# Performance work log

Hardware: AMD Instinct MI355X
Metric: run time of the kernel (lower is better)

The kernel has to match this reference:

```python
import jax, jax.numpy as jnp
import numpy as np

B, S, D, H = 2, 2048, 1024, 16
DK = D // H

def setup_inputs() -> dict:
    key = jax.random.key(0)
    ks = jax.random.split(key, 8)
    scale = 1.0 / np.sqrt(D)
    return {
        "q": jax.random.normal(ks[0], (B, S, D), jnp.float32),
        "k": jax.random.normal(ks[1], (B, S, D), jnp.float32),
        "v": jax.random.normal(ks[2], (B, S, D), jnp.float32),
        "reaches": jax.random.uniform(ks[3], (B, S), jnp.float32),
        "Wq": jax.random.normal(ks[4], (D, D), jnp.float32) * scale,
        "Wk": jax.random.normal(ks[5], (D, D), jnp.float32) * scale,
        "Wv": jax.random.normal(ks[6], (D, D), jnp.float32) * scale,
        "Wo": jax.random.normal(ks[7], (D, D), jnp.float32) * scale,
    }

def _split_heads(x):
    # [B,S,D] -> [B,H,S,DK]
    return x.reshape(B, S, H, DK).transpose(0, 2, 1, 3)

def reference(q, k, v, reaches, Wq, Wk, Wv, Wo):
    # torch Linear: y = x @ W.T
    qh = _split_heads(q @ Wq.T)
    kh = _split_heads(k @ Wk.T)
    vh = _split_heads(v @ Wv.T)
    scores = jnp.einsum("bhqd,bhkd->bhqk", qh, kh) / jnp.sqrt(jnp.float32(DK))
    scores = jax.nn.softmax(scores, axis=-1)
    # post-softmax reach weighting along key axis
    scores = scores * reaches[:, None, None, :]
    # diagonal suppression: scores - scores*0.999999*eye
    scores = scores * (1.0 - 0.999999 * jnp.eye(S, dtype=scores.dtype))
    # inverted combine
    out = vh - jnp.einsum("bhqk,bhkd->bhqd", scores, vh)
    # per-position contribution rescale
    rs = reaches.sum(axis=-1, keepdims=True)
    contrib = (rs - reaches) / (rs + 1e-9) * (1.0 - reaches) * 100.0  # [B,S]
    out = out * contrib[:, None, :, None]
    concat = out.transpose(0, 2, 1, 3).reshape(B, S, D)
    return concat @ Wo.T
```

## Files before the change

### kernel.cpp

```cpp
#include <hip/hip_runtime.h>
#include <hip/hip_bf16.h>

typedef __attribute__((ext_vector_type(8))) short short8;
typedef __attribute__((ext_vector_type(4))) float f32x4;
typedef __attribute__((ext_vector_type(16))) float f32x16;
typedef unsigned short us;

#define B_ 2
#define S_ 2048
#define D_ 1024
#define H_ 16
#define DK_ 64
#define QSCALE 0.1803368867f

__device__ __forceinline__ us f2bf(float f) {
  union { float f; unsigned u; } x; x.f = f;
  unsigned r = x.u + 0x7FFFu + ((x.u >> 16) & 1u);
  return (us)(r >> 16);
}
__device__ __forceinline__ float bf2f(us h) {
  union { unsigned u; float f; } x; x.u = ((unsigned)h) << 16;
  return x.f;
}
__device__ __forceinline__ us f2bf_hw(float f) {
  __hip_bfloat16 h = __float2bfloat16(f);
  return *reinterpret_cast<us*>(&h);
}
__device__ __forceinline__ unsigned cvtpk(float lo, float hi) {
  unsigned r;
  asm("v_cvt_pk_bf16_f32 %0, %1, %2" : "=v"(r) : "v"(lo), "v"(hi));
  return r;
}

__device__ __forceinline__ void gload16(const void* g, void* l) {
  __builtin_amdgcn_global_load_lds((const __attribute__((address_space(1))) void*)g,
                                   (__attribute__((address_space(3))) void*)l, 16, 0, 0);
}

__global__ __launch_bounds__(256) void cvt_all(const float* __restrict__ q,
                                               const float* __restrict__ k,
                                               const float* __restrict__ v,
                                               const float* __restrict__ Wq,
                                               const float* __restrict__ Wk,
                                               const float* __restrict__ Wv,
                                               const float* __restrict__ Wo,
                                               us* __restrict__ oq, us* __restrict__ ok,
                                               us* __restrict__ ov, us* __restrict__ oWq,
                                               us* __restrict__ oWk, us* __restrict__ oWv,
                                               us* __restrict__ oWo) {
  int bid = blockIdx.x;
  const float* in; us* out; int off;
  if (bid < 12288) {
    int t = bid >> 12;
    in = (t == 0) ? q : (t == 1) ? k : v;
    out = (t == 0) ? oq : (t == 1) ? ok : ov;
    off = (bid & 4095) * 1024;
  } else {
    int t = (bid - 12288) >> 10;
    in = (t == 0) ? Wq : (t == 1) ? Wk : (t == 2) ? Wv : Wo;
    out = (t == 0) ? oWq : (t == 1) ? oWk : (t == 2) ? oWv : oWo;
    off = ((bid - 12288) & 1023) * 1024;
  }
  int i = off + threadIdx.x * 4;
  float4 val = *reinterpret_cast<const float4*>(in + i);
  ushort4 o;
  o.x = f2bf(val.x); o.y = f2bf(val.y); o.z = f2bf(val.z); o.w = f2bf(val.w);
  *reinterpret_cast<ushort4*>(out + i) = o;
}

__global__ __launch_bounds__(256) void rs_kernel(const float* __restrict__ reaches,
                                                 float* __restrict__ rs) {
  int b = blockIdx.x, t = threadIdx.x;
  float s = 0.f;
  for (int i = t; i < S_; i += 256) s += reaches[b * S_ + i];
  for (int o = 32; o > 0; o >>= 1) s += __shfl_down(s, o, 64);
  __shared__ float tmp[4];
  if ((t & 63) == 0) tmp[t >> 6] = s;
  __syncthreads();
  if (t == 0) rs[b] = tmp[0] + tmp[1] + tmp[2] + tmp[3];
}

__device__ __forceinline__ void gemm_core_hs(const us* __restrict__ A, const us* __restrict__ Bt,
                                             us* __restrict__ outH, float oscale) {
  __shared__ __align__(16) us lA[3][128 * 32];
  __shared__ __align__(16) us lB[3][128 * 32];
  const int tid = threadIdx.x;
  const int bm = blockIdx.x >> 3, bn = blockIdx.x & 7;
  const int w = tid >> 6, lane = tid & 63;
  const int wr = (w >> 1) * 64, wc = (w & 1) * 64;
  const int lr = lane & 15, lg = lane >> 4;

  f32x4 acc[4][4];
#pragma unroll
  for (int i = 0; i < 4; ++i)
#pragma unroll
    for (int j = 0; j < 4; ++j) acc[i][j] = (f32x4){0.f, 0.f, 0.f, 0.f};

  const int crow = lane >> 2, ce8 = (lane & 3) * 8;
  const us* A0 = A + (size_t)(bm * 128 + w * 32 + crow) * 1024 + ce8;
  const us* A1 = A0 + (size_t)16 * 1024;
  const us* B0 = Bt + (size_t)(bn * 128 + w * 32 + crow) * 1024 + ce8;
  const us* B1 = B0 + (size_t)16 * 1024;
  const int dA0 = (w * 32) * 32, dA1 = (w * 32 + 16) * 32;

  gload16(A0, &lA[0][dA0]);
  gload16(A1, &lA[0][dA1]);
  gload16(B0, &lB[0][dA0]);
  gload16(B1, &lB[0][dA1]);

  int cur = 0, nxt = 1;
  for (int kt = 0; kt < 32; ++kt) {
    if (kt < 31) {
      int ko = (kt + 1) * 32;
      gload16(A0 + ko, &lA[nxt][dA0]);
      gload16(A1 + ko, &lA[nxt][dA1]);
      gload16(B0 + ko, &lB[nxt][dA0]);
      gload16(B1 + ko, &lB[nxt][dA1]);
      asm volatile("s_waitcnt vmcnt(4)" ::: "memory");
    } else {
      asm volatile("s_waitcnt vmcnt(0)" ::: "memory");
    }
    __builtin_amdgcn_s_barrier();
    __builtin_amdgcn_sched_barrier(0);

    short8 af[4], bfr[4];
#pragma unroll
    for (int i = 0; i < 4; ++i)
      af[i] = *reinterpret_cast<const short8*>(&lA[cur][(wr + i * 16 + lr) * 32 + lg * 8]);
#pragma unroll
    for (int j = 0; j < 4; ++j)
      bfr[j] = *reinterpret_cast<const short8*>(&lB[cur][(wc + j * 16 + lr) * 32 + lg * 8]);
    __builtin_amdgcn_s_setprio(1);
#pragma unroll
    for (int i = 0; i < 4; ++i)
#pragma unroll
      for (int j = 0; j < 4; ++j)
        acc[i][j] = __builtin_amdgcn_mfma_f32_16x16x32_bf16(af[i], bfr[j], acc[i][j], 0, 0, 0);
    __builtin_amdgcn_s_setprio(0);

    cur = nxt;
    nxt = (nxt == 2) ? 0 : nxt + 1;
  }
#pragma unroll
  for (int i = 0; i < 4; ++i)
#pragma unroll
    for (int j = 0; j < 4; ++j)
#pragma unroll
      for (int ii = 0; ii < 4; ++ii) {
        int r = bm * 128 + wr + i * 16 + lg * 4 + ii;
        int c = bn * 128 + wc + j * 16 + lr;
        float v = acc[i][j][ii] * oscale;
        int b = r >> 11, s = r & (S_ - 1), h = c >> 6, dk = c & 63;
        outH[(((size_t)(b * H_ + h) * S_ + s) * DK_) + dk] = f2bf(v);
      }
}

__global__ __launch_bounds__(256) void proj_gemm(const us* __restrict__ q_bf,
                                                 const us* __restrict__ k_bf,
                                                 const us* __restrict__ v_bf,
                                                 const us* __restrict__ Wq_bf,
                                                 const us* __restrict__ Wk_bf,
                                                 const us* __restrict__ Wv_bf,
                                                 us* __restrict__ Qh, us* __restrict__ Kh,
                                                 us* __restrict__ Vh) {
  if (blockIdx.y == 0) gemm_core_hs(q_bf, Wq_bf, Qh, QSCALE);
  else if (blockIdx.y == 1) gemm_core_hs(k_bf, Wk_bf, Kh, 1.0f);
  else gemm_core_hs(v_bf, Wv_bf, Vh, 1.0f);
}

__global__ __launch_bounds__(256) void wo_gemm(const us* __restrict__ A,
                                               const us* __restrict__ Bt,
                                               float* __restrict__ outF) {
  __shared__ __align__(16) us lA[3][128 * 32];
  __shared__ __align__(16) us lB[3][64 * 32];
  const int tid = threadIdx.x;
  const int bm = blockIdx.x >> 4, bn = blockIdx.x & 15;
  const int w = tid >> 6, lane = tid & 63;
  const int lr = lane & 15, lg = lane >> 4;

  f32x4 acc[2][4];
#pragma unroll
  for (int i = 0; i < 2; ++i)
#pragma unroll
    for (int j = 0; j < 4; ++j) acc[i][j] = (f32x4){0.f, 0.f, 0.f, 0.f};

  const int crow = lane >> 2, ce8 = (lane & 3) * 8;
  const us* A0 = A + (size_t)(bm * 128 + w * 32 + crow) * 1024 + ce8;
  const us* A1 = A0 + (size_t)16 * 1024;
  const us* B0 = Bt + (size_t)(bn * 64 + w * 16 + crow) * 1024 + ce8;
  const int dA0 = (w * 32) * 32, dA1 = (w * 32 + 16) * 32, dB0 = (w * 16) * 32;

  gload16(A0, &lA[0][dA0]);
  gload16(A1, &lA[0][dA1]);
  gload16(B0, &lB[0][dB0]);

  int cur = 0, nxt = 1;
  for (int kt = 0; kt < 32; ++kt) {
    if (kt < 31) {
      int ko = (kt + 1) * 32;
      gload16(A0 + ko, &lA[nxt][dA0]);
      gload16(A1 + ko, &lA[nxt][dA1]);
      gload16(B0 + ko, &lB[nxt][dB0]);
      asm volatile("s_waitcnt vmcnt(3)" ::: "memory");
    } else {
      asm volatile("s_waitcnt vmcnt(0)" ::: "memory");
    }
    __builtin_amdgcn_s_barrier();
    __builtin_amdgcn_sched_barrier(0);

    short8 af[2], bfr[4];
#pragma unroll
    for (int i = 0; i < 2; ++i)
      af[i] = *reinterpret_cast<const short8*>(&lA[cur][(w * 32 + i * 16 + lr) * 32 + lg * 8]);
#pragma unroll
    for (int j = 0; j < 4; ++j)
      bfr[j] = *reinterpret_cast<const short8*>(&lB[cur][(j * 16 + lr) * 32 + lg * 8]);
    __builtin_amdgcn_s_setprio(1);
#pragma unroll
    for (int i = 0; i < 2; ++i)
#pragma unroll
      for (int j = 0; j < 4; ++j)
        acc[i][j] = __builtin_amdgcn_mfma_f32_16x16x32_bf16(af[i], bfr[j], acc[i][j], 0, 0, 0);
    __builtin_amdgcn_s_setprio(0);

    cur = nxt;
    nxt = (nxt == 2) ? 0 : nxt + 1;
  }
#pragma unroll
  for (int i = 0; i < 2; ++i)
#pragma unroll
    for (int j = 0; j < 4; ++j)
#pragma unroll
      for (int ii = 0; ii < 4; ++ii) {
        int r = bm * 128 + w * 32 + i * 16 + lg * 4 + ii;
        int c = bn * 64 + j * 16 + lr;
        outF[(size_t)r * 1024 + c] = acc[i][j][ii];
      }
}

__global__ __launch_bounds__(256) void transp_kernel(const us* __restrict__ Vh,
                                                     const float* __restrict__ reaches,
                                                     us* __restrict__ VhTw) {
  __shared__ us t[64 * 68];
  const int bh = blockIdx.x >> 5, st = blockIdx.x & 31;
  const int b = bh >> 4;
  const size_t base = (size_t)bh * S_ * DK_;
  const int r = threadIdx.x >> 3, e8 = (threadIdx.x & 7) * 8;
#pragma unroll
  for (int h2 = 0; h2 < 2; ++h2) {
    int row = r + h2 * 32;
    *reinterpret_cast<short8*>(&t[row * 68 + e8]) =
        *reinterpret_cast<const short8*>(&Vh[base + (size_t)(st * 64 + row) * DK_ + e8]);
  }
  __syncthreads();
#pragma unroll
  for (int h2 = 0; h2 < 2; ++h2) {
    int dk = (threadIdx.x >> 3) + h2 * 32;
    int sc = (threadIdx.x & 7) * 8;
    short8 v;
#pragma unroll
    for (int j = 0; j < 8; ++j) {
      float rw = reaches[b * S_ + st * 64 + sc + j];
      v[j] = (short)f2bf_hw(bf2f(t[(sc + j) * 68 + dk]) * rw);
    }
    *reinterpret_cast<short8*>(&VhTw[base + (size_t)dk * S_ + st * 64 + sc]) = v;
  }
}

__global__ __launch_bounds__(256, 2) void attn_kernel(const us* __restrict__ Qh,
                                                      const us* __restrict__ Kh,
                                                      const us* __restrict__ Vh,
                                                      const us* __restrict__ VhTw,
                                                      const float* __restrict__ reaches,
                                                      const float* __restrict__ rsum,
                                                      us* __restrict__ concat) {
  __shared__ __align__(16) us sbuf[3][8192];
  __shared__ float diagP[128];
  __shared__ float lsum[128];

  const int tid = threadIdx.x;
  const int bid = ((blockIdx.x & 7) << 6) | (blockIdx.x >> 3);
  const int qt = bid & 15;
  const int bh = bid >> 4;
  const int b = bh >> 4, h = bh & 15;
  const size_t base = (size_t)bh * S_ * DK_;

  const int w = tid >> 6, lane = tid & 63;
  const int l31 = lane & 31, hh = lane >> 5, l7 = lane & 7;
  const int h4 = hh * 4;
  const int diagkt = qt * 2 + (w >> 1);

  const int Lrow = lane >> 3;
  const int cswz = (l7 ^ Lrow) << 3;
  const us* Kg0 = Kh + base + (size_t)(w * 16 + Lrow) * DK_ + cswz;
  const us* Kg1 = Kg0 + (size_t)8 * DK_;
  const us* Vg0 = VhTw + base + (size_t)(w * 16 + Lrow) * S_ + cswz;
  const us* Vg1 = Vg0 + (size_t)8 * S_;
  const int dK0 = (w * 16) * 64, dK1 = (w * 16 + 8) * 64;
  const int dV0 = 4096 + dK0, dV1 = 4096 + dK1;

  short8 aq[4];
  {
    const us* qp = &Qh[base + (size_t)(qt * 128 + w * 32 + l31) * DK_ + hh * 8];
#pragma unroll
    for (int dk = 0; dk < 4; ++dk)
      aq[dk] = *reinterpret_cast<const short8*>(qp + dk * 16);
  }

  int rdK[2][4];
#pragma unroll
  for (int c = 0; c < 2; ++c)
#pragma unroll
    for (int dk = 0; dk < 4; ++dk)
      rdK[c][dk] = (c * 32 + l31) * 64 + (((dk * 2 + hh) ^ l7) << 3);

  gload16(Kg0, &sbuf[0][dK0]);
  gload16(Kg1, &sbuf[0][dK1]);
  gload16(Vg0, &sbuf[0][dV0]);
  gload16(Vg1, &sbuf[0][dV1]);

  f32x16 oacc[2];
  float lacc = 0.f;
#pragma unroll
  for (int c = 0; c < 2; ++c)
#pragma unroll
    for (int r = 0; r < 16; ++r) oacc[c][r] = 0.f;

  int cur = 0, nxt = 1;
  for (int kt = 0; kt < 32; ++kt) {
    if (kt < 31) {
      const size_t ko = (size_t)(kt + 1) * 64;
      gload16(Kg0 + ko * DK_, &sbuf[nxt][dK0]);
      gload16(Kg1 + ko * DK_, &sbuf[nxt][dK1]);
      gload16(Vg0 + ko, &sbuf[nxt][dV0]);
      gload16(Vg1 + ko, &sbuf[nxt][dV1]);
      asm volatile("s_waitcnt vmcnt(4)" ::: "memory");
    } else {
      asm volatile("s_waitcnt vmcnt(0)" ::: "memory");
    }
    __builtin_amdgcn_s_barrier();
    __builtin_amdgcn_sched_barrier(0);

    const us* lKc = &sbuf[cur][0];
    const us* vTc = &sbuf[cur][4096];

    f32x16 st0, st1;
#pragma unroll
    for (int r = 0; r < 16; ++r) { st0[r] = 0.f; st1[r] = 0.f; }
    __builtin_amdgcn_s_setprio(1);
#pragma unroll
    for (int dk = 0; dk < 4; ++dk) {
      short8 k0 = *reinterpret_cast<const short8*>(&lKc[rdK[0][dk]]);
      st0 = __builtin_amdgcn_mfma_f32_32x32x16_bf16(k0, aq[dk], st0, 0, 0, 0);
      short8 k1 = *reinterpret_cast<const short8*>(&lKc[rdK[1][dk]]);
      st1 = __builtin_amdgcn_mfma_f32_32x32x16_bf16(k1, aq[dk], st1, 0, 0, 0);
    }
    __builtin_amdgcn_s_setprio(0);

    float e0[16], e1[16];
#pragma unroll
    for (int r = 0; r < 16; ++r) {
      e0[r] = __builtin_amdgcn_exp2f(st0[r]);
      e1[r] = __builtin_amdgcn_exp2f(st1[r]);
      lacc += e0[r] + e1[r];
    }
    if (kt == diagkt) {
#pragma unroll
      for (int r = 0; r < 16; ++r) {
        int kk = (r & 3) + 8 * (r >> 2) + 4 * hh;
        float ev = (w & 1) ? e1[r] : e0[r];
        if (kk == l31) diagP[w * 32 + l31] = ev;
      }
    }

    short8 pa[4];
#pragma unroll
    for (int ks = 0; ks < 4; ++ks) {
      const int ro = (ks & 1) * 8;
      unsigned d0, s0, d1, s1;
      if (ks < 2) {
        d0 = cvtpk(e0[ro + 0], e0[ro + 1]);
        s0 = cvtpk(e0[ro + 4], e0[ro + 5]);
        d1 = cvtpk(e0[ro + 2], e0[ro + 3]);
        s1 = cvtpk(e0[ro + 6], e0[ro + 7]);
      } else {
        d0 = cvtpk(e1[ro + 0], e1[ro + 1]);
        s0 = cvtpk(e1[ro + 4], e1[ro + 5]);
        d1 = cvtpk(e1[ro + 2], e1[ro + 3]);
        s1 = cvtpk(e1[ro + 6], e1[ro + 7]);
      }
      asm("v_permlane32_swap_b32 %0, %1" : "+v"(d0), "+v"(s0));
      asm("v_permlane32_swap_b32 %0, %1" : "+v"(d1), "+v"(s1));
      union { unsigned u[4]; short8 v; } pk;
      pk.u[0] = d0; pk.u[1] = d1; pk.u[2] = s0; pk.u[3] = s1;
      pa[ks] = pk.v;
    }

    __builtin_amdgcn_s_setprio(1);
#pragma unroll
    for (int dc = 0; dc < 2; ++dc)
#pragma unroll
      for (int ks = 0; ks < 4; ++ks) {
        short8 bv = *reinterpret_cast<const short8*>(&vTc[rdK[dc][ks]]);
        oacc[dc] = __builtin_amdgcn_mfma_f32_32x32x16_bf16(pa[ks], bv, oacc[dc], 0, 0, 0);
      }
    __builtin_amdgcn_s_setprio(0);

    cur = nxt;
    nxt = (nxt == 2) ? 0 : nxt + 1;
  }

  lacc += __shfl_xor(lacc, 32, 64);
  if (hh == 0) lsum[w * 32 + l31] = lacc;
  __syncthreads();

  const float rb = rsum[b];
#pragma unroll
  for (int r = 0; r < 16; ++r) {
    const int q = w * 32 + (r & 3) + 8 * (r >> 2) + h4;
    const int qg = qt * 128 + q;
    const float rq = reaches[b * S_ + qg];
    const float contrib = (rb - rq) / (rb + 1e-9f) * (1.f - rq) * 100.f;
    const float corr = 0.999999f * diagP[q] * rq;
    const float linv = 1.0f / lsum[q];
#pragma unroll
    for (int dc = 0; dc < 2; ++dc) {
      int d = dc * 32 + l31;
      float vhv = bf2f(Vh[base + (size_t)qg * DK_ + d]);
      float pv = (oacc[dc][r] - corr * vhv) * linv;
      float o = (vhv - pv) * contrib;
      concat[((size_t)(b * S_ + qg)) * D_ + h * 64 + d] = f2bf(o);
    }
  }
}

extern "C" void kernel_launch(void* const* d_in, const int* in_sizes, int n_in,
                              void* d_out, int out_size, void* d_ws, size_t ws_size,
                              hipStream_t stream) {
  const float* q = (const float*)d_in[0];
  const float* k = (const float*)d_in[1];
  const float* v = (const float*)d_in[2];
  const float* reaches = (const float*)d_in[3];
  const float* Wq = (const float*)d_in[4];
  const float* Wk = (const float*)d_in[5];
  const float* Wv = (const float*)d_in[6];
  const float* Wo = (const float*)d_in[7];

  const size_t NQKV = (size_t)B_ * S_ * D_;
  const size_t NW = (size_t)D_ * D_;

  us* q_bf = (us*)d_ws;
  us* k_bf = q_bf + NQKV;
  us* v_bf = k_bf + NQKV;
  us* Wq_bf = v_bf + NQKV;
  us* Wk_bf = Wq_bf + NW;
  us* Wv_bf = Wk_bf + NW;
  us* Wo_bf = Wv_bf + NW;
  us* Qh = Wo_bf + NW;
  us* Kh = Qh + NQKV;
  us* Vh = Kh + NQKV;
  us* concat = Vh + NQKV;
  float* rs = (float*)(concat + NQKV);
  us* VhTw = q_bf;

  cvt_all<<<16384, 256, 0, stream>>>(q, k, v, Wq, Wk, Wv, Wo,
                                     q_bf, k_bf, v_bf, Wq_bf, Wk_bf, Wv_bf, Wo_bf);
  rs_kernel<<<B_, 256, 0, stream>>>(reaches, rs);

  proj_gemm<<<dim3(256, 3), 256, 0, stream>>>(q_bf, k_bf, v_bf, Wq_bf, Wk_bf, Wv_bf, Qh, Kh, Vh);
  transp_kernel<<<B_ * H_ * (S_ / 64), 256, 0, stream>>>(Vh, reaches, VhTw);

  attn_kernel<<<B_ * H_ * (S_ / 128), 256, 0, stream>>>(Qh, Kh, Vh, VhTw, reaches, rs, concat);

  wo_gemm<<<512, 256, 0, stream>>>(concat, Wo_bf, (float*)d_out);
}
```

Baseline: 133.2 us.

## Fuse V transpose into projection GEMM and software-pipeline QK with softmax-PV

Measured after the change: 136.9 us. 2.8% more time.

```diff
diff --git a/kernel.cpp b/kernel.cpp
--- a/kernel.cpp
+++ b/kernel.cpp
@@ -81,9 +81,10 @@
 }
 
 __device__ __forceinline__ void gemm_core_hs(const us* __restrict__ A, const us* __restrict__ Bt,
-                                             us* __restrict__ outH, float oscale) {
-  __shared__ __align__(16) us lA[3][128 * 32];
-  __shared__ __align__(16) us lB[3][128 * 32];
+                                             us* __restrict__ outH, float oscale,
+                                             const float* __restrict__ reaches,
+                                             us* __restrict__ VhTw, int dov) {
+  __shared__ __align__(16) us smem[3][8192];
   const int tid = threadIdx.x;
   const int bm = blockIdx.x >> 3, bn = blockIdx.x & 7;
   const int w = tid >> 6, lane = tid & 63;
@@ -103,19 +104,19 @@
   const us* B1 = B0 + (size_t)16 * 1024;
   const int dA0 = (w * 32) * 32, dA1 = (w * 32 + 16) * 32;
 
-  gload16(A0, &lA[0][dA0]);
-  gload16(A1, &lA[0][dA1]);
-  gload16(B0, &lB[0][dA0]);
-  gload16(B1, &lB[0][dA1]);
+  gload16(A0, &smem[0][dA0]);
+  gload16(A1, &smem[0][dA1]);
+  gload16(B0, &smem[0][4096 + dA0]);
+  gload16(B1, &smem[0][4096 + dA1]);
 
   int cur = 0, nxt = 1;
   for (int kt = 0; kt < 32; ++kt) {
     if (kt < 31) {
       int ko = (kt + 1) * 32;
-      gload16(A0 + ko, &lA[nxt][dA0]);
-      gload16(A1 + ko, &lA[nxt][dA1]);
-      gload16(B0 + ko, &lB[nxt][dA0]);
-      gload16(B1 + ko, &lB[nxt][dA1]);
+      gload16(A0 + ko, &smem[nxt][dA0]);
+      gload16(A1 + ko, &smem[nxt][dA1]);
+      gload16(B0 + ko, &smem[nxt][4096 + dA0]);
+      gload16(B1 + ko, &smem[nxt][4096 + dA1]);
       asm volatile("s_waitcnt vmcnt(4)" ::: "memory");
     } else {
       asm volatile("s_waitcnt vmcnt(0)" ::: "memory");
@@ -126,10 +127,10 @@
     short8 af[4], bfr[4];
 #pragma unroll
     for (int i = 0; i < 4; ++i)
-      af[i] = *reinterpret_cast<const short8*>(&lA[cur][(wr + i * 16 + lr) * 32 + lg * 8]);
+      af[i] = *reinterpret_cast<const short8*>(&smem[cur][(wr + i * 16 + lr) * 32 + lg * 8]);
 #pragma unroll
     for (int j = 0; j < 4; ++j)
-      bfr[j] = *reinterpret_cast<const short8*>(&lB[cur][(wc + j * 16 + lr) * 32 + lg * 8]);
+      bfr[j] = *reinterpret_cast<const short8*>(&smem[cur][4096 + (wc + j * 16 + lr) * 32 + lg * 8]);
     __builtin_amdgcn_s_setprio(1);
 #pragma unroll
     for (int i = 0; i < 4; ++i)
@@ -141,18 +142,53 @@
     cur = nxt;
     nxt = (nxt == 2) ? 0 : nxt + 1;
   }
+
+  us* tbuf = &smem[0][0];
+  if (dov) __syncthreads();
+
 #pragma unroll
   for (int i = 0; i < 4; ++i)
 #pragma unroll
     for (int j = 0; j < 4; ++j)
 #pragma unroll
       for (int ii = 0; ii < 4; ++ii) {
-        int r = bm * 128 + wr + i * 16 + lg * 4 + ii;
-        int c = bn * 128 + wc + j * 16 + lr;
+        int rl = wr + i * 16 + lg * 4 + ii;
+        int cl = wc + j * 16 + lr;
+        int r = bm * 128 + rl;
+        int c = bn * 128 + cl;
         float v = acc[i][j][ii] * oscale;
         int b = r >> 11, s = r & (S_ - 1), h = c >> 6, dk = c & 63;
-        outH[(((size_t)(b * H_ + h) * S_ + s) * DK_) + dk] = f2bf(v);
+        us bv = f2bf(v);
+        outH[(((size_t)(b * H_ + h) * S_ + s) * DK_) + dk] = bv;
+        if (dov) tbuf[cl * 136 + rl] = bv;
       }
+
+  if (dov) {
+    __syncthreads();
+    const int dl = tid >> 1, s0q = (tid & 1) * 64;
+    const int bq = bm >> 4;
+    const int bh = bq * 16 + bn * 2 + (dl >> 6);
+    const int dk = dl & 63;
+    const int sbase = (bm & 15) * 128 + s0q;
+    const size_t ob = (size_t)bh * DK_ * S_ + (size_t)dk * S_ + sbase;
+    const float* rp = reaches + bq * S_ + sbase;
+#pragma unroll
+    for (int k8 = 0; k8 < 8; ++k8) {
+      short8 vv = *reinterpret_cast<const short8*>(&tbuf[dl * 136 + s0q + k8 * 8]);
+      float4 ra = *reinterpret_cast<const float4*>(rp + k8 * 8);
+      float4 rb = *reinterpret_cast<const float4*>(rp + k8 * 8 + 4);
+      short8 ov;
+      ov[0] = (short)f2bf_hw(bf2f((us)vv[0]) * ra.x);
+      ov[1] = (short)f2bf_hw(bf2f((us)vv[1]) * ra.y);
+      ov[2] = (short)f2bf_hw(bf2f((us)vv[2]) * ra.z);
+      ov[3] = (short)f2bf_hw(bf2f((us)vv[3]) * ra.w);
+      ov[4] = (short)f2bf_hw(bf2f((us)vv[4]) * rb.x);
+      ov[5] = (short)f2bf_hw(bf2f((us)vv[5]) * rb.y);
+      ov[6] = (short)f2bf_hw(bf2f((us)vv[6]) * rb.z);
+      ov[7] = (short)f2bf_hw(bf2f((us)vv[7]) * rb.w);
+      *reinterpret_cast<short8*>(&VhTw[ob + k8 * 8]) = ov;
+    }
+  }
 }
 
 __global__ __launch_bounds__(256) void proj_gemm(const us* __restrict__ q_bf,
@@ -162,10 +198,12 @@
                                                  const us* __restrict__ Wk_bf,
                                                  const us* __restrict__ Wv_bf,
                                                  us* __restrict__ Qh, us* __restrict__ Kh,
-                                                 us* __restrict__ Vh) {
-  if (blockIdx.y == 0) gemm_core_hs(q_bf, Wq_bf, Qh, QSCALE);
-  else if (blockIdx.y == 1) gemm_core_hs(k_bf, Wk_bf, Kh, 1.0f);
-  else gemm_core_hs(v_bf, Wv_bf, Vh, 1.0f);
+                                                 us* __restrict__ Vh,
+                                                 const float* __restrict__ reaches,
+                                                 us* __restrict__ VhTw, int dov) {
+  if (blockIdx.y == 0) gemm_core_hs(q_bf, Wq_bf, Qh, QSCALE, nullptr, nullptr, 0);
+  else if (blockIdx.y == 1) gemm_core_hs(k_bf, Wk_bf, Kh, 1.0f, nullptr, nullptr, 0);
+  else gemm_core_hs(v_bf, Wv_bf, Vh, 1.0f, reaches, VhTw, dov);
 }
 
 __global__ __launch_bounds__(256) void wo_gemm(const us* __restrict__ A,
@@ -267,6 +305,71 @@
   }
 }
 
+__device__ __forceinline__ void qk_step(const us* lKc, const int (&rdK)[2][4],
+                                        const short8 (&aq)[4], f32x16& s0, f32x16& s1) {
+#pragma unroll
+  for (int r = 0; r < 16; ++r) { s0[r] = 0.f; s1[r] = 0.f; }
+  __builtin_amdgcn_s_setprio(1);
+#pragma unroll
+  for (int dk = 0; dk < 4; ++dk) {
+    short8 k0 = *reinterpret_cast<const short8*>(&lKc[rdK[0][dk]]);
+    s0 = __builtin_amdgcn_mfma_f32_32x32x16_bf16(k0, aq[dk], s0, 0, 0, 0);
+    short8 k1 = *reinterpret_cast<const short8*>(&lKc[rdK[1][dk]]);
+    s1 = __builtin_amdgcn_mfma_f32_32x32x16_bf16(k1, aq[dk], s1, 0, 0, 0);
+  }
+  __builtin_amdgcn_s_setprio(0);
+}
+
+__device__ __forceinline__ void sm_pv_step(const f32x16& st0, const f32x16& st1, int ktv,
+                                           int diagkt, const us* vTc, const int (&rdK)[2][4],
+                                           int w, int hh, int l31, float& lacc,
+                                           f32x16& o0, f32x16& o1, float* diagP) {
+  float e0[16], e1[16];
+#pragma unroll
+  for (int r = 0; r < 16; ++r) {
+    e0[r] = __builtin_amdgcn_exp2f(st0[r]);
+    e1[r] = __builtin_amdgcn_exp2f(st1[r]);
+    lacc += e0[r] + e1[r];
+  }
+  if (ktv == diagkt) {
+#pragma unroll
+    for (int r = 0; r < 16; ++r) {
+      int kk = (r & 3) + 8 * (r >> 2) + 4 * hh;
+      float ev = (w & 1) ? e1[r] : e0[r];
+      if (kk == l31) diagP[w * 32 + l31] = ev;
+    }
+  }
+  short8 pa[4];
+#pragma unroll
+  for (int ks = 0; ks < 4; ++ks) {
+    const int ro = (ks & 1) * 8;
+    unsigned d0, s0u, d1, s1u;
+    if (ks < 2) {
+      d0 = cvtpk(e0[ro + 0], e0[ro + 1]); s0u = cvtpk(e0[ro + 4], e0[ro + 5]);
+      d1 = cvtpk(e0[ro + 2], e0[ro + 3]); s1u = cvtpk(e0[ro + 6], e0[ro + 7]);
+    } else {
+      d0 = cvtpk(e1[ro + 0], e1[ro + 1]); s0u = cvtpk(e1[ro + 4], e1[ro + 5]);
+      d1 = cvtpk(e1[ro + 2], e1[ro + 3]); s1u = cvtpk(e1[ro + 6], e1[ro + 7]);
+    }
+    asm("v_permlane32_swap_b32 %0, %1" : "+v"(d0), "+v"(s0u));
+    asm("v_permlane32_swap_b32 %0, %1" : "+v"(d1), "+v"(s1u));
+    union { unsigned u[4]; short8 v; } pk;
+    pk.u[0] = d0; pk.u[1] = d1; pk.u[2] = s0u; pk.u[3] = s1u;
+    pa[ks] = pk.v;
+  }
+  __builtin_amdgcn_s_setprio(1);
+#pragma unroll
+  for (int dc = 0; dc < 2; ++dc) {
+    f32x16& oo = dc ? o1 : o0;
+#pragma unroll
+    for (int ks = 0; ks < 4; ++ks) {
+      short8 bv = *reinterpret_cast<const short8*>(&vTc[rdK[dc][ks]]);
+      oo = __builtin_amdgcn_mfma_f32_32x32x16_bf16(pa[ks], bv, oo, 0, 0, 0);
+    }
+  }
+  __builtin_amdgcn_s_setprio(0);
+}
+
 __global__ __launch_bounds__(256, 2) void attn_kernel(const us* __restrict__ Qh,
                                                       const us* __restrict__ Kh,
                                                       const us* __restrict__ Vh,
@@ -299,6 +402,22 @@
   const int dK0 = (w * 16) * 64, dK1 = (w * 16 + 8) * 64;
   const int dV0 = 4096 + dK0, dV1 = 4096 + dK1;
 
+#define STAGE(T, BUFP)                              \
+  do {                                              \
+    const size_t ko_ = (size_t)(T) * 64;            \
+    gload16(Kg0 + ko_ * DK_, (BUFP) + dK0);         \
+    gload16(Kg1 + ko_ * DK_, (BUFP) + dK1);         \
+    gload16(Vg0 + ko_, (BUFP) + dV0);               \
+    gload16(Vg1 + ko_, (BUFP) + dV1);               \
+  } while (0)
+
+#define SYNC()                                        \
+  do {                                                \
+    asm volatile("s_waitcnt vmcnt(0)" ::: "memory");  \
+    __builtin_amdgcn_s_barrier();                     \
+    __builtin_amdgcn_sched_barrier(0);                \
+  } while (0)
+
   short8 aq[4];
   {
     const us* qp = &Qh[base + (size_t)(qt * 128 + w * 32 + l31) * DK_ + hh * 8];
@@ -314,101 +433,36 @@
     for (int dk = 0; dk < 4; ++dk)
       rdK[c][dk] = (c * 32 + l31) * 64 + (((dk * 2 + hh) ^ l7) << 3);
 
-  gload16(Kg0, &sbuf[0][dK0]);
-  gload16(Kg1, &sbuf[0][dK1]);
-  gload16(Vg0, &sbuf[0][dV0]);
-  gload16(Vg1, &sbuf[0][dV1]);
-
-  f32x16 oacc[2];
+  STAGE(0, &sbuf[0][0]);
+  STAGE(1, &sbuf[1][0]);
+  SYNC();
+
+  f32x16 oacc0, oacc1;
   float lacc = 0.f;
 #pragma unroll
-  for (int c = 0; c < 2; ++c)
-#pragma unroll
-    for (int r = 0; r < 16; ++r) oacc[c][r] = 0.f;
-
-  int cur = 0, nxt = 1;
-  for (int kt = 0; kt < 32; ++kt) {
-    if (kt < 31) {
-      const size_t ko = (size_t)(kt + 1) * 64;
-      gload16(Kg0 + ko * DK_, &sbuf[nxt][dK0]);
-      gload16(Kg1 + ko * DK_, &sbuf[nxt][dK1]);
-      gload16(Vg0 + ko, &sbuf[nxt][dV0]);
-      gload16(Vg1 + ko, &sbuf[nxt][dV1]);
-      asm volatile("s_waitcnt vmcnt(4)" ::: "memory");
-    } else {
-      asm volatile("s_waitcnt vmcnt(0)" ::: "memory");
-    }
-    __builtin_amdgcn_s_barrier();
-    __builtin_amdgcn_sched_barrier(0);
-
-    const us* lKc = &sbuf[cur][0];
-    const us* vTc = &sbuf[cur][4096];
-
-    f32x16 st0, st1;
-#pragma unroll
-    for (int r = 0; r < 16; ++r) { st0[r] = 0.f; st1[r] = 0.f; }
-    __builtin_amdgcn_s_setprio(1);
-#pragma unroll
-    for (int dk = 0; dk < 4; ++dk) {
-      short8 k0 = *reinterpret_cast<const short8*>(&lKc[rdK[0][dk]]);
-      st0 = __builtin_amdgcn_mfma_f32_32x32x16_bf16(k0, aq[dk], st0, 0, 0, 0);
-      short8 k1 = *reinterpret_cast<const short8*>(&lKc[rdK[1][dk]]);
-      st1 = __builtin_amdgcn_mfma_f32_32x32x16_bf16(k1, aq[dk], st1, 0, 0, 0);
-    }
-    __builtin_amdgcn_s_setprio(0);
-
-    float e0[16], e1[16];
-#pragma unroll
-    for (int r = 0; r < 16; ++r) {
-      e0[r] = __builtin_amdgcn_exp2f(st0[r]);
-      e1[r] = __builtin_amdgcn_exp2f(st1[r]);
-      lacc += e0[r] + e1[r];
-    }
-    if (kt == diagkt) {
-#pragma unroll
-      for (int r = 0; r < 16; ++r) {
-        int kk = (r & 3) + 8 * (r >> 2) + 4 * hh;
-        float ev = (w & 1) ? e1[r] : e0[r];
-        if (kk == l31) diagP[w * 32 + l31] = ev;
-      }
-    }
-
-    short8 pa[4];
-#pragma unroll
-    for (int ks = 0; ks < 4; ++ks) {
-      const int ro = (ks & 1) * 8;
-      unsigned d0, s0, d1, s1;
-      if (ks < 2) {
-        d0 = cvtpk(e0[ro + 0], e0[ro + 1]);
-        s0 = cvtpk(e0[ro + 4], e0[ro + 5]);
-        d1 = cvtpk(e0[ro + 2], e0[ro + 3]);
-        s1 = cvtpk(e0[ro + 6], e0[ro + 7]);
-      } else {
-        d0 = cvtpk(e1[ro + 0], e1[ro + 1]);
-        s0 = cvtpk(e1[ro + 4], e1[ro + 5]);
-        d1 = cvtpk(e1[ro + 2], e1[ro + 3]);
-        s1 = cvtpk(e1[ro + 6], e1[ro + 7]);
-      }
-      asm("v_permlane32_swap_b32 %0, %1" : "+v"(d0), "+v"(s0));
-      asm("v_permlane32_swap_b32 %0, %1" : "+v"(d1), "+v"(s1));
-      union { unsigned u[4]; short8 v; } pk;
-      pk.u[0] = d0; pk.u[1] = d1; pk.u[2] = s0; pk.u[3] = s1;
-      pa[ks] = pk.v;
-    }
-
-    __builtin_amdgcn_s_setprio(1);
-#pragma unroll
-    for (int dc = 0; dc < 2; ++dc)
-#pragma unroll
-      for (int ks = 0; ks < 4; ++ks) {
-        short8 bv = *reinterpret_cast<const short8*>(&vTc[rdK[dc][ks]]);
-        oacc[dc] = __builtin_amdgcn_mfma_f32_32x32x16_bf16(pa[ks], bv, oacc[dc], 0, 0, 0);
-      }
-    __builtin_amdgcn_s_setprio(0);
-
-    cur = nxt;
-    nxt = (nxt == 2) ? 0 : nxt + 1;
-  }
+  for (int r = 0; r < 16; ++r) { oacc0[r] = 0.f; oacc1[r] = 0.f; }
+
+  f32x16 stA0, stA1, stB0, stB1;
+  qk_step(&sbuf[0][0], rdK, aq, stA0, stA1);
+
+  int cur = 0, nx1 = 1, nx2 = 2;
+  for (int kt = 0; kt < 32; kt += 2) {
+    if (kt + 2 < 32) STAGE(kt + 2, &sbuf[nx2][0]);
+    qk_step(&sbuf[nx1][0], rdK, aq, stB0, stB1);
+    sm_pv_step(stA0, stA1, kt, diagkt, &sbuf[cur][4096], rdK, w, hh, l31,
+               lacc, oacc0, oacc1, diagP);
+    SYNC();
+    { int t = cur; cur = nx1; nx1 = nx2; nx2 = t; }
+
+    if (kt + 3 < 32) STAGE(kt + 3, &sbuf[nx2][0]);
+    if (kt + 2 < 32) qk_step(&sbuf[nx1][0], rdK, aq, stA0, stA1);
+    sm_pv_step(stB0, stB1, kt + 1, diagkt, &sbuf[cur][4096], rdK, w, hh, l31,
+               lacc, oacc0, oacc1, diagP);
+    if (kt + 1 < 31) SYNC();
+    { int t = cur; cur = nx1; nx1 = nx2; nx2 = t; }
+  }
+#undef STAGE
+#undef SYNC
 
   lacc += __shfl_xor(lacc, 32, 64);
   if (hh == 0) lsum[w * 32 + l31] = lacc;
@@ -427,7 +481,8 @@
     for (int dc = 0; dc < 2; ++dc) {
       int d = dc * 32 + l31;
       float vhv = bf2f(Vh[base + (size_t)qg * DK_ + d]);
-      float pv = (oacc[dc][r] - corr * vhv) * linv;
+      float oaccv = dc ? oacc1[r] : oacc0[r];
+      float pv = (oaccv - corr * vhv) * linv;
       float o = (vhv - pv) * contrib;
       concat[((size_t)(b * S_ + qg)) * D_ + h * 64 + d] = f2bf(o);
     }
@@ -461,14 +516,20 @@
   us* Vh = Kh + NQKV;
   us* concat = Vh + NQKV;
   float* rs = (float*)(concat + NQKV);
-  us* VhTw = q_bf;
+
+  us* vt_new = (us*)(rs + 4);
+  size_t need = (size_t)((char*)(vt_new + NQKV) - (char*)d_ws);
+  int fused = (ws_size >= need) ? 1 : 0;
+  us* VhTw = fused ? vt_new : q_bf;
 
   cvt_all<<<16384, 256, 0, stream>>>(q, k, v, Wq, Wk, Wv, Wo,
                                      q_bf, k_bf, v_bf, Wq_bf, Wk_bf, Wv_bf, Wo_bf);
   rs_kernel<<<B_, 256, 0, stream>>>(reaches, rs);
 
-  proj_gemm<<<dim3(256, 3), 256, 0, stream>>>(q_bf, k_bf, v_bf, Wq_bf, Wk_bf, Wv_bf, Qh, Kh, Vh);
-  transp_kernel<<<B_ * H_ * (S_ / 64), 256, 0, stream>>>(Vh, reaches, VhTw);
+  proj_gemm<<<dim3(256, 3), 256, 0, stream>>>(q_bf, k_bf, v_bf, Wq_bf, Wk_bf, Wv_bf,
+                                              Qh, Kh, Vh, reaches, VhTw, fused);
+  if (!fused)
+    transp_kernel<<<B_ * H_ * (S_ / 64), 256, 0, stream>>>(Vh, reaches, VhTw);
 
   attn_kernel<<<B_ * H_ * (S_ / 128), 256, 0, stream>>>(Qh, Kh, Vh, VhTw, reaches, rs, concat);
 
```

## Split attention keys across wave pairs with 64-row query tiles; fold row-sum into convert

Applied to the files above, without the earlier changes.

After: 139.3 us. 1.05x slower.

```diff
diff --git a/kernel.cpp b/kernel.cpp
--- a/kernel.cpp
+++ b/kernel.cpp
@@ -44,11 +44,26 @@
                                                const float* __restrict__ Wk,
                                                const float* __restrict__ Wv,
                                                const float* __restrict__ Wo,
+                                               const float* __restrict__ reaches,
                                                us* __restrict__ oq, us* __restrict__ ok,
                                                us* __restrict__ ov, us* __restrict__ oWq,
                                                us* __restrict__ oWk, us* __restrict__ oWv,
-                                               us* __restrict__ oWo) {
+                                               us* __restrict__ oWo, float* __restrict__ rs) {
   int bid = blockIdx.x;
+  if (bid >= 16384) {
+    __shared__ float tmp[4];
+    int t = threadIdx.x;
+    for (int b = 0; b < B_; ++b) {
+      float s = 0.f;
+      for (int i = t; i < S_; i += 256) s += reaches[b * S_ + i];
+      for (int o = 32; o > 0; o >>= 1) s += __shfl_down(s, o, 64);
+      if ((t & 63) == 0) tmp[t >> 6] = s;
+      __syncthreads();
+      if (t == 0) rs[b] = tmp[0] + tmp[1] + tmp[2] + tmp[3];
+      __syncthreads();
+    }
+    return;
+  }
   const float* in; us* out; int off;
   if (bid < 12288) {
     int t = bid >> 12;
@@ -68,18 +83,6 @@
   *reinterpret_cast<ushort4*>(out + i) = o;
 }
 
-__global__ __launch_bounds__(256) void rs_kernel(const float* __restrict__ reaches,
-                                                 float* __restrict__ rs) {
-  int b = blockIdx.x, t = threadIdx.x;
-  float s = 0.f;
-  for (int i = t; i < S_; i += 256) s += reaches[b * S_ + i];
-  for (int o = 32; o > 0; o >>= 1) s += __shfl_down(s, o, 64);
-  __shared__ float tmp[4];
-  if ((t & 63) == 0) tmp[t >> 6] = s;
-  __syncthreads();
-  if (t == 0) rs[b] = tmp[0] + tmp[1] + tmp[2] + tmp[3];
-}
-
 __device__ __forceinline__ void gemm_core_hs(const us* __restrict__ A, const us* __restrict__ Bt,
                                              us* __restrict__ outH, float oscale) {
   __shared__ __align__(16) us lA[3][128 * 32];
@@ -267,128 +270,112 @@
   }
 }
 
-__global__ __launch_bounds__(256, 2) void attn_kernel(const us* __restrict__ Qh,
+__global__ __launch_bounds__(256, 4) void attn_kernel(const us* __restrict__ Qh,
                                                       const us* __restrict__ Kh,
                                                       const us* __restrict__ Vh,
                                                       const us* __restrict__ VhTw,
                                                       const float* __restrict__ reaches,
                                                       const float* __restrict__ rsum,
                                                       us* __restrict__ concat) {
-  __shared__ __align__(16) us sbuf[3][8192];
-  __shared__ float diagP[128];
-  __shared__ float lsum[128];
+  __shared__ __align__(16) us sbuf[4][4096];
+  __shared__ float diagP[64];
+  __shared__ float lown[64];
+  __shared__ float lpart[64];
+  float* mscr = reinterpret_cast<float*>(&sbuf[0][0]);
 
   const int tid = threadIdx.x;
-  const int bid = ((blockIdx.x & 7) << 6) | (blockIdx.x >> 3);
-  const int qt = bid & 15;
-  const int bh = bid >> 4;
+  const int bid = ((blockIdx.x & 7) << 7) | (blockIdx.x >> 3);
+  const int qt = bid & 31;
+  const int bh = bid >> 5;
   const int b = bh >> 4, h = bh & 15;
   const size_t base = (size_t)bh * S_ * DK_;
 
   const int w = tid >> 6, lane = tid & 63;
+  const int wq = w >> 1, wk = w & 1;
   const int l31 = lane & 31, hh = lane >> 5, l7 = lane & 7;
   const int h4 = hh * 4;
-  const int diagkt = qt * 2 + (w >> 1);
-
-  const int Lrow = lane >> 3;
-  const int cswz = (l7 ^ Lrow) << 3;
-  const us* Kg0 = Kh + base + (size_t)(w * 16 + Lrow) * DK_ + cswz;
-  const us* Kg1 = Kg0 + (size_t)8 * DK_;
-  const us* Vg0 = VhTw + base + (size_t)(w * 16 + Lrow) * S_ + cswz;
-  const us* Vg1 = Vg0 + (size_t)8 * S_;
-  const int dK0 = (w * 16) * 64, dK1 = (w * 16 + 8) * 64;
-  const int dV0 = 4096 + dK0, dV1 = 4096 + dK1;
+  const int r2 = tid >> 3, e8 = (tid & 7) * 8;
 
   short8 aq[4];
   {
-    const us* qp = &Qh[base + (size_t)(qt * 128 + w * 32 + l31) * DK_ + hh * 8];
+    const us* qp = &Qh[base + (size_t)(qt * 64 + wq * 32 + l31) * DK_ + hh * 8];
 #pragma unroll
     for (int dk = 0; dk < 4; ++dk)
       aq[dk] = *reinterpret_cast<const short8*>(qp + dk * 16);
   }
 
-  int rdK[2][4];
-#pragma unroll
-  for (int c = 0; c < 2; ++c)
-#pragma unroll
-    for (int dk = 0; dk < 4; ++dk)
-      rdK[c][dk] = (c * 32 + l31) * 64 + (((dk * 2 + hh) ^ l7) << 3);
-
-  gload16(Kg0, &sbuf[0][dK0]);
-  gload16(Kg1, &sbuf[0][dK1]);
-  gload16(Vg0, &sbuf[0][dV0]);
-  gload16(Vg1, &sbuf[0][dV1]);
-
-  f32x16 oacc[2];
+  int rdK[4], rdV[2][2];
+#pragma unroll
+  for (int dk = 0; dk < 4; ++dk)
+    rdK[dk] = (wk * 32 + l31) * 64 + (((dk * 2 + hh) ^ l7) << 3);
+#pragma unroll
+  for (int dc = 0; dc < 2; ++dc)
+#pragma unroll
+    for (int ks = 0; ks < 2; ++ks)
+      rdV[dc][ks] = (dc * 32 + l31) * 64 + (((wk * 4 + ks * 2 + hh) ^ l7) << 3);
+
+  const int wslot = ((tid & 7) ^ (r2 & 7)) << 3;
+  const int wK0 = r2 * 64 + wslot, wK1 = (r2 + 32) * 64 + wslot;
+
+  short8 pk0, pk1, pv0, pv1;
+  pk0 = *reinterpret_cast<const short8*>(&Kh[base + (size_t)r2 * DK_ + e8]);
+  pk1 = *reinterpret_cast<const short8*>(&Kh[base + (size_t)(r2 + 32) * DK_ + e8]);
+  pv0 = *reinterpret_cast<const short8*>(&VhTw[base + (size_t)r2 * S_ + e8]);
+  pv1 = *reinterpret_cast<const short8*>(&VhTw[base + (size_t)(r2 + 32) * S_ + e8]);
+  *reinterpret_cast<short8*>(&sbuf[0][wK0]) = pk0;
+  *reinterpret_cast<short8*>(&sbuf[0][wK1]) = pk1;
+  *reinterpret_cast<short8*>(&sbuf[2][wK0]) = pv0;
+  *reinterpret_cast<short8*>(&sbuf[2][wK1]) = pv1;
+  __syncthreads();
+
+  f32x16 oacc0, oacc1;
   float lacc = 0.f;
 #pragma unroll
-  for (int c = 0; c < 2; ++c)
-#pragma unroll
-    for (int r = 0; r < 16; ++r) oacc[c][r] = 0.f;
-
-  int cur = 0, nxt = 1;
+  for (int r = 0; r < 16; ++r) { oacc0[r] = 0.f; oacc1[r] = 0.f; }
+
   for (int kt = 0; kt < 32; ++kt) {
+    const int cur = kt & 1;
     if (kt < 31) {
-      const size_t ko = (size_t)(kt + 1) * 64;
-      gload16(Kg0 + ko * DK_, &sbuf[nxt][dK0]);
-      gload16(Kg1 + ko * DK_, &sbuf[nxt][dK1]);
-      gload16(Vg0 + ko, &sbuf[nxt][dV0]);
-      gload16(Vg1 + ko, &sbuf[nxt][dV1]);
-      asm volatile("s_waitcnt vmcnt(4)" ::: "memory");
-    } else {
-      asm volatile("s_waitcnt vmcnt(0)" ::: "memory");
-    }
-    __builtin_amdgcn_s_barrier();
-    __builtin_amdgcn_sched_barrier(0);
-
-    const us* lKc = &sbuf[cur][0];
-    const us* vTc = &sbuf[cur][4096];
-
-    f32x16 st0, st1;
-#pragma unroll
-    for (int r = 0; r < 16; ++r) { st0[r] = 0.f; st1[r] = 0.f; }
+      int nt = kt + 1;
+      pk0 = *reinterpret_cast<const short8*>(&Kh[base + (size_t)(nt * 64 + r2) * DK_ + e8]);
+      pk1 = *reinterpret_cast<const short8*>(&Kh[base + (size_t)(nt * 64 + r2 + 32) * DK_ + e8]);
+      pv0 = *reinterpret_cast<const short8*>(&VhTw[base + (size_t)r2 * S_ + nt * 64 + e8]);
+      pv1 = *reinterpret_cast<const short8*>(&VhTw[base + (size_t)(r2 + 32) * S_ + nt * 64 + e8]);
+    }
+
+    f32x16 st;
+#pragma unroll
+    for (int r = 0; r < 16; ++r) st[r] = 0.f;
     __builtin_amdgcn_s_setprio(1);
 #pragma unroll
     for (int dk = 0; dk < 4; ++dk) {
-      short8 k0 = *reinterpret_cast<const short8*>(&lKc[rdK[0][dk]]);
-      st0 = __builtin_amdgcn_mfma_f32_32x32x16_bf16(k0, aq[dk], st0, 0, 0, 0);
-      short8 k1 = *reinterpret_cast<const short8*>(&lKc[rdK[1][dk]]);
-      st1 = __builtin_amdgcn_mfma_f32_32x32x16_bf16(k1, aq[dk], st1, 0, 0, 0);
+      short8 k0 = *reinterpret_cast<const short8*>(&sbuf[cur][rdK[dk]]);
+      st = __builtin_amdgcn_mfma_f32_32x32x16_bf16(k0, aq[dk], st, 0, 0, 0);
     }
     __builtin_amdgcn_s_setprio(0);
 
-    float e0[16], e1[16];
+    float e[16];
 #pragma unroll
     for (int r = 0; r < 16; ++r) {
-      e0[r] = __builtin_amdgcn_exp2f(st0[r]);
-      e1[r] = __builtin_amdgcn_exp2f(st1[r]);
-      lacc += e0[r] + e1[r];
-    }
-    if (kt == diagkt) {
+      e[r] = __builtin_amdgcn_exp2f(st[r]);
+      lacc += e[r];
+    }
+    if (kt == qt && wq == wk) {
 #pragma unroll
       for (int r = 0; r < 16; ++r) {
-        int kk = (r & 3) + 8 * (r >> 2) + 4 * hh;
-        float ev = (w & 1) ? e1[r] : e0[r];
-        if (kk == l31) diagP[w * 32 + l31] = ev;
+        int kk = (r & 3) + 8 * (r >> 2) + h4;
+        if (kk == l31) diagP[wq * 32 + l31] = e[r];
       }
     }
 
-    short8 pa[4];
-#pragma unroll
-    for (int ks = 0; ks < 4; ++ks) {
-      const int ro = (ks & 1) * 8;
-      unsigned d0, s0, d1, s1;
-      if (ks < 2) {
-        d0 = cvtpk(e0[ro + 0], e0[ro + 1]);
-        s0 = cvtpk(e0[ro + 4], e0[ro + 5]);
-        d1 = cvtpk(e0[ro + 2], e0[ro + 3]);
-        s1 = cvtpk(e0[ro + 6], e0[ro + 7]);
-      } else {
-        d0 = cvtpk(e1[ro + 0], e1[ro + 1]);
-        s0 = cvtpk(e1[ro + 4], e1[ro + 5]);
-        d1 = cvtpk(e1[ro + 2], e1[ro + 3]);
-        s1 = cvtpk(e1[ro + 6], e1[ro + 7]);
-      }
+    short8 pa[2];
+#pragma unroll
+    for (int ks = 0; ks < 2; ++ks) {
+      const int ro = ks * 8;
+      unsigned d0 = cvtpk(e[ro + 0], e[ro + 1]);
+      unsigned s0 = cvtpk(e[ro + 4], e[ro + 5]);
+      unsigned d1 = cvtpk(e[ro + 2], e[ro + 3]);
+      unsigned s1 = cvtpk(e[ro + 6], e[ro + 7]);
       asm("v_permlane32_swap_b32 %0, %1" : "+v"(d0), "+v"(s0));
       asm("v_permlane32_swap_b32 %0, %1" : "+v"(d1), "+v"(s1));
       union { unsigned u[4]; short8 v; } pk;
@@ -398,38 +385,59 @@
 
     __builtin_amdgcn_s_setprio(1);
 #pragma unroll
-    for (int dc = 0; dc < 2; ++dc)
-#pragma unroll
-      for (int ks = 0; ks < 4; ++ks) {
-        short8 bv = *reinterpret_cast<const short8*>(&vTc[rdK[dc][ks]]);
-        oacc[dc] = __builtin_amdgcn_mfma_f32_32x32x16_bf16(pa[ks], bv, oacc[dc], 0, 0, 0);
+    for (int ks = 0; ks < 2; ++ks) {
+      short8 bv0 = *reinterpret_cast<const short8*>(&sbuf[2 + cur][rdV[0][ks]]);
+      oacc0 = __builtin_amdgcn_mfma_f32_32x32x16_bf16(pa[ks], bv0, oacc0, 0, 0, 0);
+      short8 bv1 = *reinterpret_cast<const short8*>(&sbuf[2 + cur][rdV[1][ks]]);
+      oacc1 = __builtin_amdgcn_mfma_f32_32x32x16_bf16(pa[ks], bv1, oacc1, 0, 0, 0);
+    }
+    __builtin_amdgcn_s_setprio(0);
+
+    if (kt < 31) {
+      const int nx = cur ^ 1;
+      *reinterpret_cast<short8*>(&sbuf[nx][wK0]) = pk0;
+      *reinterpret_cast<short8*>(&sbuf[nx][wK1]) = pk1;
+      *reinterpret_cast<short8*>(&sbuf[2 + nx][wK0]) = pv0;
+      *reinterpret_cast<short8*>(&sbuf[2 + nx][wK1]) = pv1;
+    }
+    __syncthreads();
+  }
+
+  lacc += __shfl_xor(lacc, 32, 64);
+  __syncthreads();
+
+  if (wk == 1) {
+#pragma unroll
+    for (int r = 0; r < 16; ++r) {
+      int q = wq * 32 + (r & 3) + 8 * (r >> 2) + h4;
+      mscr[q * 64 + l31] = oacc0[r];
+      mscr[q * 64 + 32 + l31] = oacc1[r];
+    }
+    if (hh == 0) lpart[wq * 32 + l31] = lacc;
+  } else {
+    if (hh == 0) lown[wq * 32 + l31] = lacc;
+  }
+  __syncthreads();
+
+  if (wk == 0) {
+    const float rb = rsum[b];
+#pragma unroll
+    for (int r = 0; r < 16; ++r) {
+      const int q = wq * 32 + (r & 3) + 8 * (r >> 2) + h4;
+      const int qg = qt * 64 + q;
+      const float rq = reaches[b * S_ + qg];
+      const float contrib = (rb - rq) / (rb + 1e-9f) * (1.f - rq) * 100.f;
+      const float corr = 0.999999f * diagP[q] * rq;
+      const float linv = 1.0f / (lown[q] + lpart[q]);
+#pragma unroll
+      for (int dc = 0; dc < 2; ++dc) {
+        int d = dc * 32 + l31;
+        float vhv = bf2f(Vh[base + (size_t)qg * DK_ + d]);
+        float oaccv = (dc ? oacc1[r] : oacc0[r]) + mscr[q * 64 + d];
+        float pv = (oaccv - corr * vhv) * linv;
+        float o = (vhv - pv) * contrib;
+        concat[((size_t)(b * S_ + qg)) * D_ + h * 64 + d] = f2bf(o);
       }
-    __builtin_amdgcn_s_setprio(0);
-
-    cur = nxt;
-    nxt = (nxt == 2) ? 0 : nxt + 1;
-  }
-
-  lacc += __shfl_xor(lacc, 32, 64);
-  if (hh == 0) lsum[w * 32 + l31] = lacc;
-  __syncthreads();
-
-  const float rb = rsum[b];
-#pragma unroll
-  for (int r = 0; r < 16; ++r) {
-    const int q = w * 32 + (r & 3) + 8 * (r >> 2) + h4;
-    const int qg = qt * 128 + q;
-    const float rq = reaches[b * S_ + qg];
-    const float contrib = (rb - rq) / (rb + 1e-9f) * (1.f - rq) * 100.f;
-    const float corr = 0.999999f * diagP[q] * rq;
-    const float linv = 1.0f / lsum[q];
-#pragma unroll
-    for (int dc = 0; dc < 2; ++dc) {
-      int d = dc * 32 + l31;
-      float vhv = bf2f(Vh[base + (size_t)qg * DK_ + d]);
-      float pv = (oacc[dc][r] - corr * vhv) * linv;
-      float o = (vhv - pv) * contrib;
-      concat[((size_t)(b * S_ + qg)) * D_ + h * 64 + d] = f2bf(o);
     }
   }
 }
@@ -463,14 +471,13 @@
   float* rs = (float*)(concat + NQKV);
   us* VhTw = q_bf;
 
-  cvt_all<<<16384, 256, 0, stream>>>(q, k, v, Wq, Wk, Wv, Wo,
-                                     q_bf, k_bf, v_bf, Wq_bf, Wk_bf, Wv_bf, Wo_bf);
-  rs_kernel<<<B_, 256, 0, stream>>>(reaches, rs);
+  cvt_all<<<16385, 256, 0, stream>>>(q, k, v, Wq, Wk, Wv, Wo, reaches,
+                                     q_bf, k_bf, v_bf, Wq_bf, Wk_bf, Wv_bf, Wo_bf, rs);
 
   proj_gemm<<<dim3(256, 3), 256, 0, stream>>>(q_bf, k_bf, v_bf, Wq_bf, Wk_bf, Wv_bf, Qh, Kh, Vh);
   transp_kernel<<<B_ * H_ * (S_ / 64), 256, 0, stream>>>(Vh, reaches, VhTw);
 
-  attn_kernel<<<B_ * H_ * (S_ / 128), 256, 0, stream>>>(Qh, Kh, Vh, VhTw, reaches, rs, concat);
+  attn_kernel<<<B_ * H_ * (S_ / 64), 256, 0, stream>>>(Qh, Kh, Vh, VhTw, reaches, rs, concat);
 
   wo_gemm<<<512, 256, 0, stream>>>(concat, Wo_bf, (float*)d_out);
 }
```
